# Optimization experiments

Measured on AMD Instinct MI355X. Metric: run time of the kernel, lower is better.

Reference implementation:

```python
import jax, jax.numpy as jnp
from jax import lax
import numpy as np

N_HEADS, N_FEATURES, IMG_W, IMG_H, C_DOWN = 8, 64, 96, 96, 32


def setup_inputs() -> dict:
    key = jax.random.key(0)
    ks = jax.random.split(key, 16)
    d = {
        'X': jax.random.normal(ks[0], (N_FEATURES, IMG_W, IMG_H), jnp.float32),
        'WQ_task': jax.random.normal(ks[1], (N_HEADS, N_FEATURES, 1, 1), jnp.float32),
        'BQ_task': jax.random.normal(ks[2], (N_HEADS, N_FEATURES, 1, 1), jnp.float32),
        'WK_task': jax.random.normal(ks[3], (N_FEATURES, 1, 1), jnp.float32),
        'BK_task': jax.random.normal(ks[4], (N_FEATURES, 1, 1), jnp.float32),
        'WV_task': jax.random.normal(ks[5], (1, C_DOWN, 1, 1), jnp.float32),
        'BV_task': jax.random.normal(ks[6], (1, C_DOWN, 1, 1), jnp.float32),
        # learned parameters (loaded from disk in the original)
        'WQ_t_minus_1': jax.random.uniform(ks[7], (N_HEADS, N_FEATURES, 1, 1), jnp.float32),
        'WQ_x': jax.random.uniform(ks[8], (1, N_FEATURES, 1, 1), jnp.float32),
        'BQ': jax.random.uniform(ks[9], (N_HEADS, N_FEATURES, 1, 1), jnp.float32),
        'WK_x': jax.random.uniform(ks[10], (N_FEATURES, 1, 1), jnp.float32),
        'BK': jax.random.uniform(ks[11], (N_FEATURES, 1, 1), jnp.float32),
        'Vconv_w': jax.random.normal(ks[12], (C_DOWN, N_FEATURES, 3, 3), jnp.float32) * 0.05,
        'Vconv_b': jax.random.normal(ks[13], (C_DOWN,), jnp.float32) * 0.05,
        # recurrent state (zeros at t=0 in original; random here to exercise the path)
        'prev_Q': jax.random.normal(ks[14], (N_HEADS, N_FEATURES, IMG_W, IMG_H), jnp.float32),
    }
    return d


def reference(X, WQ_task, BQ_task, WK_task, BK_task, WV_task, BV_task,
              WQ_t_minus_1, WQ_x, BQ, WK_x, BK, Vconv_w, Vconv_b, prev_Q):
    F, W, H = X.shape
    rx = X[None]  # (1, F, W, H)
    # Q: (A, F, W, H);  K: (F, W, H)
    Q = WQ_task * jax.nn.relu(WQ_t_minus_1 * prev_Q + WQ_x * rx + BQ) + BQ_task
    K = WK_task * jax.nn.relu(WK_x * X + BK) + BK_task
    # similarity[w,h,u,v] = sum_{a,f} Q[a,f,w,h] * K[f,u,v]
    #                     = sum_f (sum_a Q)[f,w,h] * K[f,u,v]  -> a (WH,F)@(F,WH) GEMM
    Qs = Q.sum(axis=0)  # (F, W, H)
    sim = jnp.einsum('fwh,fuv->whuv', Qs, K)  # (W, H, W, H)
    attn = jax.nn.softmax(sim.reshape(W, H, W * H), axis=-1)  # (W, H, WH)
    # V = task-modulated 3x3 conv of X
    Vc = lax.conv_general_dilated(rx, Vconv_w, window_strides=(1, 1), padding='SAME',
                                  dimension_numbers=('NCHW', 'OIHW', 'NCHW'))
    Vc = Vc + Vconv_b[None, :, None, None]
    V = (WV_task * Vc + BV_task)[0].reshape(C_DOWN, W * H)  # (C, WH)
    # out[c,w,h] = sum_k attn[w,h,k] * V[c,k]
    out = jnp.einsum('whk,ck->cwh', attn, V)  # (C, W, H)
    return out
```

## Files before the change

### kernel.cpp

```cpp
#include <hip/hip_runtime.h>

#define WH 9216
#define NF 64
#define NC 32
#define NH 8
#define IMGW 96
#define IMGH 96
#define PW 98
#define PPLANE 9604
#define L2E 1.4426950408889634f
#define DEFER 11.5f

typedef float f32x4 __attribute__((ext_vector_type(4)));
typedef short short8 __attribute__((ext_vector_type(8)));

__device__ inline short bf16_bits(float x) {
  __bf16 h = (__bf16)x;
  return __builtin_bit_cast(short, h);
}
__device__ inline float bf16_round(float x) { return (float)(__bf16)x; }

__global__ __launch_bounds__(256, 2) void pad_wpack_kernel(
    const float* __restrict__ X, const float* __restrict__ Wc,
    const float* __restrict__ WV_task,
    unsigned short* __restrict__ padXT, short8* __restrict__ wfrag)
{
  const int bid = blockIdx.x;
  const int t = threadIdx.x;
  if (bid < 301) {
    const int idx = bid * 256 + t;
    if (idx < 76832) {
      const int fi = idx / PPLANE;
      const int p = idx - fi * PPLANE;
      const int pw = p / PW;
      const int ph = p - pw * PW;
      short8 r;
      if (pw >= 1 && pw <= IMGW && ph >= 1 && ph <= IMGH) {
        const float* src = X + (size_t)fi * 8 * WH + (pw - 1) * IMGH + (ph - 1);
        #pragma unroll
        for (int e = 0; e < 8; ++e) r[e] = bf16_bits(src[(size_t)e * WH]);
      } else {
        #pragma unroll
        for (int e = 0; e < 8; ++e) r[e] = 0;
      }
      *(short8*)&padXT[(size_t)p * 64 + fi * 8] = r;
    }
  } else {
    #pragma unroll
    for (int j = 0; j < 9; ++j) {
      const int ridx = j * 256 + t;
      const int ct = ridx / 1152;
      const int rem = ridx - ct * 1152;
      const int cc = rem >> 6;
      const int lane = rem & 63;
      const int c = ct * 16 + (lane & 15);
      const int tap = cc >> 1;
      const int f0 = (cc & 1) * 32 + 8 * (lane >> 4);
      const float wv = WV_task[c];
      short8 r;
      #pragma unroll
      for (int e = 0; e < 8; ++e)
        r[e] = bf16_bits(wv * Wc[((size_t)c * NF + f0 + e) * 9 + tap]);
      wfrag[ridx] = r;
    }
  }
}

__global__ __launch_bounds__(256, 2) void qsk_vconv_kernel(
    const float* __restrict__ X, const float* __restrict__ WQ_task,
    const float* __restrict__ BQ_task, const float* __restrict__ WK_task,
    const float* __restrict__ BK_task, const float* __restrict__ WQ_t1,
    const float* __restrict__ WQ_x, const float* __restrict__ BQ,
    const float* __restrict__ WK_x, const float* __restrict__ BK,
    const float* __restrict__ prevQ,
    const unsigned short* __restrict__ padXT, const short8* __restrict__ wfrag,
    const float* __restrict__ bc, const float* __restrict__ WV_task,
    const float* __restrict__ BV_task,
    short* __restrict__ qfrag, short* __restrict__ kfrag,
    short* __restrict__ vfrag)
{
  __shared__ float Vt[2][32][20];
  const int bid = blockIdx.x;
  const int t = threadIdx.x;
  const int lane = t & 63;
  const int h = lane >> 4;
  if (bid < 576) {
    const int w2 = t >> 6;
    const int fh = w2 & 1, sub = w2 >> 1;
    const int T = bid;
    const int wh = T * 16 + (lane & 15);
    const int f0 = fh * 32 + 8 * h + 4 * sub;

    float x[4];
    #pragma unroll
    for (int e = 0; e < 4; ++e) x[e] = X[(size_t)(f0 + e) * WH + wh];
    float pq[32];
    #pragma unroll
    for (int a = 0; a < NH; ++a)
      #pragma unroll
      for (int e = 0; e < 4; ++e)
        pq[a * 4 + e] = prevQ[(size_t)(a * 64 + f0 + e) * WH + wh];

    const float4 wkx = *(const float4*)&WK_x[f0];
    const float4 bk  = *(const float4*)&BK[f0];
    const float4 wkt = *(const float4*)&WK_task[f0];
    const float4 bkt = *(const float4*)&BK_task[f0];
    const float4 wqx = *(const float4*)&WQ_x[f0];

    float q[4], k[4], xq[4];
    k[0] = fmaf(wkt.x, fmaxf(fmaf(wkx.x, x[0], bk.x), 0.f), bkt.x);
    k[1] = fmaf(wkt.y, fmaxf(fmaf(wkx.y, x[1], bk.y), 0.f), bkt.y);
    k[2] = fmaf(wkt.z, fmaxf(fmaf(wkx.z, x[2], bk.z), 0.f), bkt.z);
    k[3] = fmaf(wkt.w, fmaxf(fmaf(wkx.w, x[3], bk.w), 0.f), bkt.w);
    xq[0] = wqx.x * x[0]; xq[1] = wqx.y * x[1];
    xq[2] = wqx.z * x[2]; xq[3] = wqx.w * x[3];
    q[0] = q[1] = q[2] = q[3] = 0.f;
    #pragma unroll
    for (int a = 0; a < NH; ++a) {
      const int af0 = a * 64 + f0;
      const float4 w1  = *(const float4*)&WQ_t1[af0];
      const float4 bq  = *(const float4*)&BQ[af0];
      const float4 wqt = *(const float4*)&WQ_task[af0];
      const float4 bqt = *(const float4*)&BQ_task[af0];
      q[0] = fmaf(wqt.x, fmaxf(fmaf(w1.x, pq[a * 4 + 0], xq[0] + bq.x), 0.f), q[0]) + bqt.x;
      q[1] = fmaf(wqt.y, fmaxf(fmaf(w1.y, pq[a * 4 + 1], xq[1] + bq.y), 0.f), q[1]) + bqt.y;
      q[2] = fmaf(wqt.z, fmaxf(fmaf(w1.z, pq[a * 4 + 2], xq[2] + bq.z), 0.f), q[2]) + bqt.z;
      q[3] = fmaf(wqt.w, fmaxf(fmaf(w1.w, pq[a * 4 + 3], xq[3] + bq.w), 0.f), q[3]) + bqt.w;
    }

    short4 qh, ql, kh, klo;
    {
      float qs0 = q[0] * L2E, qs1 = q[1] * L2E, qs2 = q[2] * L2E, qs3 = q[3] * L2E;
      qh.x = bf16_bits(qs0); ql.x = bf16_bits(qs0 - bf16_round(qs0));
      qh.y = bf16_bits(qs1); ql.y = bf16_bits(qs1 - bf16_round(qs1));
      qh.z = bf16_bits(qs2); ql.z = bf16_bits(qs2 - bf16_round(qs2));
      qh.w = bf16_bits(qs3); ql.w = bf16_bits(qs3 - bf16_round(qs3));
      kh.x = bf16_bits(k[0]); klo.x = bf16_bits(k[0] - bf16_round(k[0]));
      kh.y = bf16_bits(k[1]); klo.y = bf16_bits(k[1] - bf16_round(k[1]));
      kh.z = bf16_bits(k[2]); klo.z = bf16_bits(k[2] - bf16_round(k[2]));
      kh.w = bf16_bits(k[3]); klo.w = bf16_bits(k[3] - bf16_round(k[3]));
    }
    const size_t offh = ((size_t)(T * 4 + fh) * 64 + lane) * 8 + sub * 4;
    const size_t offl = ((size_t)(T * 4 + 2 + fh) * 64 + lane) * 8 + sub * 4;
    *(short4*)&qfrag[offh] = qh;
    *(short4*)&qfrag[offl] = ql;
    *(short4*)&kfrag[offh] = kh;
    *(short4*)&kfrag[offl] = klo;
  } else {
    const int ktile = bid - 576;
    const int w = t >> 6;
    const int half = w & 1, ct = w >> 1;
    const int key = ktile * 16 + (lane & 15);
    const int kw = key / IMGH, kh = key - kw * IMGH;

    f32x4 acc = {0.f, 0.f, 0.f, 0.f};
    #pragma unroll
    for (int i = 0; i < 9; ++i) {
      const int cc = half * 9 + i;
      const int tap = cc >> 1;
      const int di = tap / 3, dj = tap - di * 3;
      const int f0 = (cc & 1) * 32 + 8 * h;
      const int sp = (kw + di) * PW + (kh + dj);
      const short8 xf = *(const short8*)&padXT[(size_t)sp * 64 + f0];
      acc = __builtin_amdgcn_mfma_f32_16x16x32_bf16(wfrag[(size_t)(ct * 18 + cc) * 64 + lane],
                                                    xf, acc, 0, 0, 0);
    }
    #pragma unroll
    for (int reg = 0; reg < 4; ++reg)
      Vt[half][ct * 16 + 4 * h + reg][lane & 15] = acc[reg];
    __syncthreads();
    if (t < 128) {
      const int ct2 = t >> 6;
      const int c = ct2 * 16 + (lane & 15);
      const float bias = fmaf(WV_task[c], bc[c], BV_task[c]);
      short4 r;
      #pragma unroll
      for (int j = 0; j < 4; ++j) {
        const int kl = 4 * h + j;
        r[j] = bf16_bits(Vt[0][c][kl] + Vt[1][c][kl] + bias);
      }
      const int chh = ktile >> 1, eh = ktile & 1;
      *(short4*)&vfrag[(((size_t)chh * 2 + ct2) * 64 + lane) * 8 + eh * 4] = r;
    }
  }
}

__global__ __launch_bounds__(256, 3) void flash_mfma(
    const short8* __restrict__ qfrag, const short8* __restrict__ kfrag,
    const short8* __restrict__ vfrag, float* __restrict__ part, int cps)
{
  __shared__ float red[4][3][16][34];
  const int t = threadIdx.x;
  const int lane = t & 63, wave = t >> 6;
  const int h = lane >> 4;
  const int qb = blockIdx.x;
  const int s = blockIdx.y;

  short8 qf[3][4];
  #pragma unroll
  for (int g = 0; g < 3; ++g)
    #pragma unroll
    for (int tm = 0; tm < 4; ++tm)
      qf[g][tm] = qfrag[((size_t)(qb * 3 + g) * 4 + tm) * 64 + lane];

  f32x4 acc[2][3];
  #pragma unroll
  for (int ct = 0; ct < 2; ++ct)
    #pragma unroll
    for (int g = 0; g < 3; ++g)
      acc[ct][g] = (f32x4){0.f, 0.f, 0.f, 0.f};
  float m[3] = {0.f, 0.f, 0.f};
  float l[3] = {0.f, 0.f, 0.f};

  const int cpw = cps >> 2;
  const int ch0 = s * cps + wave;
  #pragma unroll 2
  for (int it = 0; it < cpw; ++it) {
    const int ch = ch0 + it * 4;
    short8 kf[2][4];
    #pragma unroll
    for (int kt = 0; kt < 2; ++kt)
      #pragma unroll
      for (int tm = 0; tm < 4; ++tm)
        kf[kt][tm] = kfrag[((size_t)(2 * ch + kt) * 4 + tm) * 64 + lane];
    const short8 vf0 = vfrag[(size_t)(ch * 2 + 0) * 64 + lane];
    const short8 vf1 = vfrag[(size_t)(ch * 2 + 1) * 64 + lane];

    f32x4 st[3][2];
    __builtin_amdgcn_s_setprio(1);
    #pragma unroll
    for (int g = 0; g < 3; ++g) {
      const float nm = -m[g];
      f32x4 a0 = {nm, nm, nm, nm};
      f32x4 a1 = a0;
      a0 = __builtin_amdgcn_mfma_f32_16x16x32_bf16(kf[0][0], qf[g][0], a0, 0, 0, 0);
      a0 = __builtin_amdgcn_mfma_f32_16x16x32_bf16(kf[0][1], qf[g][1], a0, 0, 0, 0);
      a0 = __builtin_amdgcn_mfma_f32_16x16x32_bf16(kf[0][2], qf[g][0], a0, 0, 0, 0);
      a0 = __builtin_amdgcn_mfma_f32_16x16x32_bf16(kf[0][3], qf[g][1], a0, 0, 0, 0);
      a0 = __builtin_amdgcn_mfma_f32_16x16x32_bf16(kf[0][0], qf[g][2], a0, 0, 0, 0);
      a0 = __builtin_amdgcn_mfma_f32_16x16x32_bf16(kf[0][1], qf[g][3], a0, 0, 0, 0);
      a1 = __builtin_amdgcn_mfma_f32_16x16x32_bf16(kf[1][0], qf[g][0], a1, 0, 0, 0);
      a1 = __builtin_amdgcn_mfma_f32_16x16x32_bf16(kf[1][1], qf[g][1], a1, 0, 0, 0);
      a1 = __builtin_amdgcn_mfma_f32_16x16x32_bf16(kf[1][2], qf[g][0], a1, 0, 0, 0);
      a1 = __builtin_amdgcn_mfma_f32_16x16x32_bf16(kf[1][3], qf[g][1], a1, 0, 0, 0);
      a1 = __builtin_amdgcn_mfma_f32_16x16x32_bf16(kf[1][0], qf[g][2], a1, 0, 0, 0);
      a1 = __builtin_amdgcn_mfma_f32_16x16x32_bf16(kf[1][1], qf[g][3], a1, 0, 0, 0);
      st[g][0] = a0;
      st[g][1] = a1;
    }
    __builtin_amdgcn_s_setprio(0);

    short8 pb[3];
    #pragma unroll
    for (int g = 0; g < 3; ++g) {
      f32x4 st0 = st[g][0], st1 = st[g][1];
      const float loc = fmaxf(fmaxf(fmaxf(st0[0], st0[1]), fmaxf(st0[2], st0[3])),
                              fmaxf(fmaxf(st1[0], st1[1]), fmaxf(st1[2], st1[3])));
      if (__any(loc > DEFER)) {
        float tr = loc;
        tr = fmaxf(tr, __shfl_xor(tr, 16));
        tr = fmaxf(tr, __shfl_xor(tr, 32));
        const float d = fmaxf(tr, 0.f);
        const float r = exp2f(-d);
        l[g] *= r;
        acc[0][g] *= r;
        acc[1][g] *= r;
        m[g] += d;
        #pragma unroll
        for (int e = 0; e < 4; ++e) { st0[e] -= d; st1[e] -= d; }
      }
      float p0[4], p1[4];
      #pragma unroll
      for (int e = 0; e < 4; ++e) {
        p0[e] = exp2f(st0[e]);
        p1[e] = exp2f(st1[e]);
        pb[g][e] = bf16_bits(p0[e]);
        pb[g][4 + e] = bf16_bits(p1[e]);
      }
      l[g] += ((p0[0] + p0[1]) + (p0[2] + p0[3])) + ((p1[0] + p1[1]) + (p1[2] + p1[3]));
    }

    __builtin_amdgcn_s_setprio(1);
    #pragma unroll
    for (int g = 0; g < 3; ++g) {
      acc[0][g] = __builtin_amdgcn_mfma_f32_16x16x32_bf16(vf0, pb[g], acc[0][g], 0, 0, 0);
      acc[1][g] = __builtin_amdgcn_mfma_f32_16x16x32_bf16(vf1, pb[g], acc[1][g], 0, 0, 0);
    }
    __builtin_amdgcn_s_setprio(0);
  }

  const int q16 = lane & 15;
  #pragma unroll
  for (int g = 0; g < 3; ++g) {
    float lf = l[g] + __shfl_xor(l[g], 16);
    lf += __shfl_xor(lf, 32);
    #pragma unroll
    for (int e = 0; e < 4; ++e) {
      red[wave][g][q16][4 * h + e] = acc[0][g][e];
      red[wave][g][q16][16 + 4 * h + e] = acc[1][g][e];
    }
    if (h == 0) { red[wave][g][q16][32] = m[g]; red[wave][g][q16][33] = lf; }
  }
  __syncthreads();

  if (t < 192) {
    const int q = t & 15;
    const int g = (t >> 4) % 3;
    const int c0 = (t / 48) * 8;
    const float m0 = red[0][g][q][32], m1 = red[1][g][q][32];
    const float m2 = red[2][g][q][32], m3 = red[3][g][q][32];
    const float M = fmaxf(fmaxf(m0, m1), fmaxf(m2, m3));
    const float w0 = exp2f(m0 - M), w1 = exp2f(m1 - M);
    const float w2 = exp2f(m2 - M), w3 = exp2f(m3 - M);
    const int qg = qb * 48 + g * 16 + q;
    float* base = part + ((size_t)s * WH + qg) * 36;
    #pragma unroll
    for (int c = 0; c < 8; ++c) {
      const float A = w0 * red[0][g][q][c0 + c] + w1 * red[1][g][q][c0 + c]
                    + w2 * red[2][g][q][c0 + c] + w3 * red[3][g][q][c0 + c];
      __builtin_nontemporal_store(A, base + c0 + c);
    }
    if (c0 == 0) {
      const float L = w0 * red[0][g][q][33] + w1 * red[1][g][q][33]
                    + w2 * red[2][g][q][33] + w3 * red[3][g][q][33];
      __builtin_nontemporal_store(M, base + 32);
      __builtin_nontemporal_store(L, base + 33);
    }
  }
}

__global__ __launch_bounds__(256) void merge_kernel(
    const float* __restrict__ part, float* __restrict__ out, int units)
{
  const int t = threadIdx.x;
  const int cl = t & 31;
  const int wh = blockIdx.x * 8 + (t >> 5);
  float M = -1e30f, L = 0.f, A = 0.f;
  for (int u = 0; u < units; ++u) {
    const float* base = part + ((size_t)u * WH + wh) * 36;
    const float mu = __builtin_nontemporal_load(base + 32);
    const float lu = __builtin_nontemporal_load(base + 33);
    const float au = __builtin_nontemporal_load(base + cl);
    if (mu > M) {
      const float sc = exp2f(M - mu);
      L = fmaf(L, sc, lu);
      A = fmaf(A, sc, au);
      M = mu;
    } else {
      const float e = exp2f(mu - M);
      L = fmaf(e, lu, L);
      A = fmaf(e, au, A);
    }
  }
  out[(size_t)cl * WH + wh] = A / L;
}

extern "C" void kernel_launch(void* const* d_in, const int* in_sizes, int n_in,
                              void* d_out, int out_size, void* d_ws, size_t ws_size,
                              hipStream_t stream)
{
  const float* X   = (const float*)d_in[0];
  const float* WQt = (const float*)d_in[1];
  const float* BQt = (const float*)d_in[2];
  const float* WKt = (const float*)d_in[3];
  const float* BKt = (const float*)d_in[4];
  const float* WVt = (const float*)d_in[5];
  const float* BVt = (const float*)d_in[6];
  const float* WQ1 = (const float*)d_in[7];
  const float* WQx = (const float*)d_in[8];
  const float* BQ  = (const float*)d_in[9];
  const float* WKx = (const float*)d_in[10];
  const float* BK  = (const float*)d_in[11];
  const float* Wc  = (const float*)d_in[12];
  const float* bc  = (const float*)d_in[13];
  const float* pQ  = (const float*)d_in[14];
  float* out = (float*)d_out;

  short8* qfrag = (short8*)d_ws;
  short8* kfrag = qfrag + (size_t)147456;
  short8* vfrag = kfrag + (size_t)147456;
  short8* wfrag = vfrag + (size_t)36864;
  unsigned short* padXT = (unsigned short*)(wfrag + 2304);
  float* part = (float*)((char*)padXT + (size_t)PPLANE * 64 * 2);
  const size_t base_bytes = ((size_t)147456 * 2 + 36864 + 2304) * 16 + (size_t)PPLANE * 64 * 2;

  int ksplit = 8;
  while (ksplit > 1 &&
         base_bytes + (size_t)ksplit * WH * 36 * sizeof(float) > ws_size)
    ksplit >>= 1;
  const int cps = 288 / ksplit;
  const int units = ksplit;

  pad_wpack_kernel<<<dim3(302), 256, 0, stream>>>(X, Wc, WVt, padXT, wfrag);
  qsk_vconv_kernel<<<dim3(1152), 256, 0, stream>>>(X, WQt, BQt, WKt, BKt,
                                                   WQ1, WQx, BQ, WKx, BK, pQ,
                                                   padXT, wfrag, bc, WVt, BVt,
                                                   (short*)qfrag, (short*)kfrag,
                                                   (short*)vfrag);
  flash_mfma<<<dim3(192, ksplit), 256, 0, stream>>>(qfrag, kfrag, vfrag, part, cps);
  merge_kernel<<<dim3(WH / 8), 256, 0, stream>>>(part, out, units);
}
```

Measured before the change: 82.32 us.

## Compute softmax row sums via ones-MFMA and merge rescale check across groups

The softmax denominator is no longer built from per-lane scalar adds of fp32 probabilities. It is now accumulated by an extra MFMA that multiplies a ones-fragment by the bf16 probability fragment, which moves VALU work onto the matrix unit and drops the final cross-lane shuffles for l. The rescale check is hoisted so one __any vote covers all three query groups instead of three. bf16 packing now uses the v_cvt_pk_bf16_f32 instruction directly. The row sum is now computed from bf16-rounded probabilities, which matches the numerator rounding but costs one extra MFMA per group per chunk.

After: 82.77 us. No clear change (+0.5%).

```diff
diff --git a/kernel.cpp b/kernel.cpp
--- a/kernel.cpp
+++ b/kernel.cpp
@@ -13,12 +13,16 @@
 
 typedef float f32x4 __attribute__((ext_vector_type(4)));
 typedef short short8 __attribute__((ext_vector_type(8)));
+typedef int int4v __attribute__((ext_vector_type(4)));
 
 __device__ inline short bf16_bits(float x) {
   __bf16 h = (__bf16)x;
   return __builtin_bit_cast(short, h);
 }
 __device__ inline float bf16_round(float x) { return (float)(__bf16)x; }
+__device__ inline float fmax3(float a, float b, float c) {
+  return fmaxf(fmaxf(a, b), c);
+}
 
 __global__ __launch_bounds__(256, 2) void pad_wpack_kernel(
     const float* __restrict__ X, const float* __restrict__ Wc,
@@ -203,14 +207,22 @@
     for (int tm = 0; tm < 4; ++tm)
       qf[g][tm] = qfrag[((size_t)(qb * 3 + g) * 4 + tm) * 64 + lane];
 
+  short8 onesA = {0, 0, 0, 0, 0, 0, 0, 0};
+  if ((lane & 15) == 0) {
+    const short ob = bf16_bits(1.0f);
+    #pragma unroll
+    for (int e = 0; e < 8; ++e) onesA[e] = ob;
+  }
+
   f32x4 acc[2][3];
+  f32x4 acc2[3];
   #pragma unroll
-  for (int ct = 0; ct < 2; ++ct)
-    #pragma unroll
-    for (int g = 0; g < 3; ++g)
-      acc[ct][g] = (f32x4){0.f, 0.f, 0.f, 0.f};
+  for (int g = 0; g < 3; ++g) {
+    acc[0][g] = (f32x4){0.f, 0.f, 0.f, 0.f};
+    acc[1][g] = (f32x4){0.f, 0.f, 0.f, 0.f};
+    acc2[g]   = (f32x4){0.f, 0.f, 0.f, 0.f};
+  }
   float m[3] = {0.f, 0.f, 0.f};
-  float l[3] = {0.f, 0.f, 0.f};
 
   const int cpw = cps >> 2;
   const int ch0 = s * cps + wave;
@@ -250,34 +262,46 @@
     }
     __builtin_amdgcn_s_setprio(0);
 
-    short8 pb[3];
+    float gmax[3];
     #pragma unroll
     for (int g = 0; g < 3; ++g) {
-      f32x4 st0 = st[g][0], st1 = st[g][1];
-      const float loc = fmaxf(fmaxf(fmaxf(st0[0], st0[1]), fmaxf(st0[2], st0[3])),
-                              fmaxf(fmaxf(st1[0], st1[1]), fmaxf(st1[2], st1[3])));
-      if (__any(loc > DEFER)) {
-        float tr = loc;
+      float t0 = fmax3(st[g][0][0], st[g][0][1], st[g][0][2]);
+      t0 = fmax3(t0, st[g][0][3], st[g][1][0]);
+      t0 = fmax3(t0, st[g][1][1], st[g][1][2]);
+      gmax[g] = fmaxf(t0, st[g][1][3]);
+    }
+    if (__any(fmax3(gmax[0], gmax[1], gmax[2]) > DEFER)) {
+      #pragma unroll
+      for (int g = 0; g < 3; ++g) {
+        float tr = gmax[g];
         tr = fmaxf(tr, __shfl_xor(tr, 16));
         tr = fmaxf(tr, __shfl_xor(tr, 32));
         const float d = fmaxf(tr, 0.f);
         const float r = exp2f(-d);
-        l[g] *= r;
         acc[0][g] *= r;
         acc[1][g] *= r;
+        acc2[g] *= r;
         m[g] += d;
         #pragma unroll
-        for (int e = 0; e < 4; ++e) { st0[e] -= d; st1[e] -= d; }
+        for (int e = 0; e < 4; ++e) { st[g][0][e] -= d; st[g][1][e] -= d; }
       }
-      float p0[4], p1[4];
+    }
+    short8 pb[3];
+    #pragma unroll
+    for (int g = 0; g < 3; ++g) {
+      float p[8];
       #pragma unroll
       for (int e = 0; e < 4; ++e) {
-        p0[e] = exp2f(st0[e]);
-        p1[e] = exp2f(st1[e]);
-        pb[g][e] = bf16_bits(p0[e]);
-        pb[g][4 + e] = bf16_bits(p1[e]);
+        p[e] = exp2f(st[g][0][e]);
+        p[4 + e] = exp2f(st[g][1][e]);
       }
-      l[g] += ((p0[0] + p0[1]) + (p0[2] + p0[3])) + ((p1[0] + p1[1]) + (p1[2] + p1[3]));
+      int w0, w1, w2, w3;
+      asm("v_cvt_pk_bf16_f32 %0, %1, %2" : "=v"(w0) : "v"(p[0]), "v"(p[1]));
+      asm("v_cvt_pk_bf16_f32 %0, %1, %2" : "=v"(w1) : "v"(p[2]), "v"(p[3]));
+      asm("v_cvt_pk_bf16_f32 %0, %1, %2" : "=v"(w2) : "v"(p[4]), "v"(p[5]));
+      asm("v_cvt_pk_bf16_f32 %0, %1, %2" : "=v"(w3) : "v"(p[6]), "v"(p[7]));
+      const int4v wi = {w0, w1, w2, w3};
+      pb[g] = __builtin_bit_cast(short8, wi);
     }
 
     __builtin_amdgcn_s_setprio(1);
@@ -285,6 +309,7 @@
     for (int g = 0; g < 3; ++g) {
       acc[0][g] = __builtin_amdgcn_mfma_f32_16x16x32_bf16(vf0, pb[g], acc[0][g], 0, 0, 0);
       acc[1][g] = __builtin_amdgcn_mfma_f32_16x16x32_bf16(vf1, pb[g], acc[1][g], 0, 0, 0);
+      acc2[g]   = __builtin_amdgcn_mfma_f32_16x16x32_bf16(onesA, pb[g], acc2[g], 0, 0, 0);
     }
     __builtin_amdgcn_s_setprio(0);
   }
@@ -292,14 +317,12 @@
   const int q16 = lane & 15;
   #pragma unroll
   for (int g = 0; g < 3; ++g) {
-    float lf = l[g] + __shfl_xor(l[g], 16);
-    lf += __shfl_xor(lf, 32);
     #pragma unroll
     for (int e = 0; e < 4; ++e) {
       red[wave][g][q16][4 * h + e] = acc[0][g][e];
       red[wave][g][q16][16 + 4 * h + e] = acc[1][g][e];
     }
-    if (h == 0) { red[wave][g][q16][32] = m[g]; red[wave][g][q16][33] = lf; }
+    if (h == 0) { red[wave][g][q16][32] = m[g]; red[wave][g][q16][33] = acc2[g][0]; }
   }
   __syncthreads();
 
```
